# Kernel tuning notes

Hardware: AMD Instinct MI355X
Metric: run time of the kernel (lower is better)

## Reference

```python
import jax, jax.numpy as jnp
import numpy as np
from math import sqrt

ALPHA = 1.0
EPS = 1e-8


def setup_inputs() -> dict:
    key = jax.random.key(0)
    k1, k2, k3 = jax.random.split(key, 3)
    B, L, S, H, E = 4, 2048, 2048, 16, 64
    queries = jax.random.normal(k1, (B, L, H, E), dtype=jnp.float32)
    keys = jax.random.normal(k2, (B, S, H, E), dtype=jnp.float32)
    values = jax.random.normal(k3, (B, S, H, E), dtype=jnp.float32)
    return {"queries": queries, "keys": keys, "values": values}


def reference(queries, keys, values):
    B, L, H, E = queries.shape
    scale = 1.0 / sqrt(E)
    # dot product scores: [B,H,L,S]
    dot = jnp.einsum('blhe,bshe->bhls', queries, keys)
    # squared norms: [B,H,L,1] and [B,H,1,S]
    qn2 = jnp.sum(queries * queries, axis=-1).transpose(0, 2, 1)[..., :, None]
    kn2 = jnp.sum(keys * keys, axis=-1).transpose(0, 2, 1)[..., None, :]
    # wedge (parallelogram area) norm^2 = |q|^2|k|^2 - (q.k)^2, clipped at 0
    wedge_norm = jnp.sqrt(jax.nn.relu(qn2 * kn2 - dot * dot) + EPS)
    scores = ((1.0 - ALPHA) * dot + ALPHA * wedge_norm) * scale
    A = jax.nn.softmax(scores, axis=-1)  # no mask (mask_flag=False), dropout=0
    V = jnp.einsum('bhls,bshd->blhd', A, values)
    return V, jnp.mean(jnp.abs(scores))
```

## Files before the change

kernel.cpp:

```cpp
#include <hip/hip_runtime.h>
#include <math.h>

constexpr int Bb = 4, Ll = 2048, Ss = 2048, Hh = 16, Ee = 64;
constexpr float SCALE = 0.125f;
constexpr float EPSV  = 1e-8f;
constexpr float S2E   = 0.125f * 1.44269504089f;
constexpr float INV_CNT = 1.0f / (4.0f * 16.0f * 2048.0f * 2048.0f);

typedef __attribute__((ext_vector_type(8))) short  short8;
typedef __attribute__((ext_vector_type(4))) float  floatx4;

#define MFMA __builtin_amdgcn_mfma_f32_16x16x32_bf16

#define GLL(gp, lp)                                                        \
  __builtin_amdgcn_global_load_lds(                                        \
      (const __attribute__((address_space(1))) unsigned int*)(gp),         \
      (__attribute__((address_space(3))) unsigned int*)(lp), 16, 0, 0)

__device__ __forceinline__ short f2bf(float f) {
  unsigned u = __builtin_bit_cast(unsigned, f);
  u += 0x7fffu + ((u >> 16) & 1u);
  return (short)(u >> 16);
}
__device__ __forceinline__ float sq4(float4 v) {
  return v.x * v.x + v.y * v.y + v.z * v.z + v.w * v.w;
}
__device__ __forceinline__ short8 pack8(float4 x, float4 y) {
  short8 r;
  r[0] = f2bf(x.x); r[1] = f2bf(x.y); r[2] = f2bf(x.z); r[3] = f2bf(x.w);
  r[4] = f2bf(y.x); r[5] = f2bf(y.y); r[6] = f2bf(y.z); r[7] = f2bf(y.w);
  return r;
}

__global__ __launch_bounds__(256) void geom_pre_kernel(
    const float* __restrict__ Kg, const float* __restrict__ Vg,
    short* __restrict__ Kbf, short* __restrict__ Vtg,
    float* __restrict__ kn2g, float* __restrict__ sumg) {
  __shared__ short Vl[64][72];
  const int tid = threadIdx.x;
  const int bid = blockIdx.x;
  const int st = bid & 31, h = (bid >> 5) & 15, b = bid >> 9;
  const int s0 = st * 64;
  const int r64 = tid >> 2, ec = (tid & 3) * 16;
  const int bh = b * 16 + h;

  if (bid == 0 && tid == 0) *sumg = 0.0f;

  const float4* kp = (const float4*)(Kg + (((size_t)b * Ss + s0 + r64) * Hh + h) * Ee + ec);
  float4 k0 = kp[0], k1 = kp[1], k2 = kp[2], k3 = kp[3];
  float kn = sq4(k0) + sq4(k1) + sq4(k2) + sq4(k3);
  kn += __shfl_xor(kn, 1);
  kn += __shfl_xor(kn, 2);
  if ((tid & 3) == 0) kn2g[(size_t)bh * Ss + s0 + r64] = kn;
  short* ko = Kbf + ((size_t)bh * Ss + s0 + r64) * Ee + ec;
  *(short8*)(ko)     = pack8(k0, k1);
  *(short8*)(ko + 8) = pack8(k2, k3);

  const float4* vp = (const float4*)(Vg + (((size_t)b * Ss + s0 + r64) * Hh + h) * Ee + ec);
  float4 v0 = vp[0], v1 = vp[1], v2 = vp[2], v3 = vp[3];
  *(short8*)(&Vl[r64][ec])     = pack8(v0, v1);
  *(short8*)(&Vl[r64][ec + 8]) = pack8(v2, v3);
  __syncthreads();
  const int e = tid >> 2, sc = (tid & 3) * 16;
  short8 t0, t1;
#pragma unroll
  for (int j = 0; j < 8; ++j) {
    t0[j] = Vl[sc + j][e];
    t1[j] = Vl[sc + 8 + j][e];
  }
  short* vo = Vtg + ((size_t)bh * Ee + e) * Ss + s0 + sc;
  *(short8*)(vo)     = t0;
  *(short8*)(vo + 8) = t1;
}

constexpr int VOFF = 8192, POFF = 16384, KNOFF = 25600, LWOFF = 33792, RDOFF = 34048;

__global__ __launch_bounds__(256, 4) void geom_attn_kernel(
    const float* __restrict__ Qg, const short* __restrict__ Kbf,
    const short* __restrict__ Vtg, const float* __restrict__ kn2g,
    float* __restrict__ outg, float* __restrict__ sumg) {
  __shared__ __align__(16) char smem[34064];

  const int tid  = threadIdx.x;
  const int w    = tid >> 6;
  const int lane = tid & 63;
  const int c    = lane & 15;
  const int q4   = lane >> 4;

  const int bid = blockIdx.x;
  const int lt = bid & 31, h = (bid >> 5) & 15, b = bid >> 9;
  const int l0 = lt * 64 + w * 16;
  const int bh = b * 16 + h;

  const float4* qp = (const float4*)(Qg + (((size_t)b * Ll + (l0 + c)) * Hh + h) * Ee);
  float4 a0 = qp[2 * q4], a1 = qp[2 * q4 + 1];
  float4 a2 = qp[8 + 2 * q4], a3 = qp[9 + 2 * q4];
  float qn = sq4(a0) + sq4(a1) + sq4(a2) + sq4(a3);
  qn += __shfl_xor(qn, 16);
  qn += __shfl_xor(qn, 32);
  const float qn2v = qn;
  short8 qb0 = pack8(a0, a1);
  short8 qb1 = pack8(a2, a3);

  const int Gl = w * 128 + lane;
  const int rK = Gl >> 3, pK = Gl & 7;
  const int gK = pK ^ (rK & 7);
  const char* kSrc = (const char*)Kbf + (size_t)bh * Ss * 128 + rK * 128 + gK * 16;
  const char* vSrc = (const char*)Vtg + (size_t)bh * Ee * 4096 + rK * 4096 + gK * 16;
  char* kDst = smem + w * 2048;
  char* vDst = smem + VOFF + w * 2048;

  {
    const char* knSrc = (const char*)kn2g + (size_t)bh * 8192 + (w * 128 + lane) * 16;
    char* knDst = smem + KNOFF + w * 2048;
    GLL(knSrc, knDst);
    GLL(knSrc + 1024, knDst + 1024);
  }

  const int addrA0 = c * 128 + ((q4 ^ (c & 7)) << 4);
  const int addrA1 = addrA0 ^ 64;
  const char* pKa0 = smem + addrA0;
  const char* pKa1 = smem + addrA1;
  char* pPw  = smem + POFF + w * 2304;
  char* pPwr = pPw + c * 144 + q4 * 8;
  const char* pPrd = pPw + c * 144;
  const char* pKn  = smem + KNOFF + q4 * 16;
  float* lw = (float*)(smem + LWOFF + w * 64);
  float* red = (float*)(smem + RDOFF);

  floatx4 o0 = {0.f, 0.f, 0.f, 0.f}, o1 = o0, o2 = o0, o3 = o0;
  float lp = 0.0f, scsum = 0.0f;

  for (int s0 = 0; s0 < Ss; s0 += 64) {
    __syncthreads();
    GLL(kSrc, kDst);
    GLL(kSrc + 1024, kDst + 1024);
    GLL(vSrc, vDst);
    GLL(vSrc + 32768, vDst + 1024);
    kSrc += 8192;
    vSrc += 128;
    __syncthreads();

#pragma unroll
    for (int ct = 0; ct < 4; ++ct) {
      short8 ka0 = *(const short8*)(pKa0 + ct * 2048);
      short8 ka1 = *(const short8*)(pKa1 + ct * 2048);
      floatx4 d = {0.f, 0.f, 0.f, 0.f};
      d = MFMA(ka0, qb0, d, 0, 0, 0);
      d = MFMA(ka1, qb1, d, 0, 0, 0);
      float4 knv = *(const float4*)(pKn + s0 * 4 + ct * 64);
      float p[4];
#pragma unroll
      for (int r = 0; r < 4; ++r) {
        float dot = d[r];
        float w2 = fmaf(-dot, dot, qn2v * (&knv.x)[r]);
        w2 = fmaxf(w2, 0.0f) + EPSV;
        float rt = __builtin_amdgcn_sqrtf(w2);
        scsum += rt * SCALE;
        float pe = __builtin_amdgcn_exp2f(rt * S2E);
        lp += pe;
        p[r] = pe;
      }
      unsigned u0 = __builtin_bit_cast(unsigned, p[0]) + 0x8000u;
      unsigned u1 = __builtin_bit_cast(unsigned, p[1]) + 0x8000u;
      unsigned u2 = __builtin_bit_cast(unsigned, p[2]) + 0x8000u;
      unsigned u3 = __builtin_bit_cast(unsigned, p[3]) + 0x8000u;
      uint2 pk;
      pk.x = __builtin_amdgcn_perm(u1, u0, 0x07060302u);
      pk.y = __builtin_amdgcn_perm(u3, u2, 0x07060302u);
      *(uint2*)(pPwr + ct * 32) = pk;
    }

#pragma unroll
    for (int kc = 0; kc < 2; ++kc) {
      short8 pa = *(const short8*)(pPrd + kc * 64);
      const char* vb = (kc == 0 ? pKa0 : pKa1) + VOFF;
      short8 v0 = *(const short8*)(vb);
      short8 v1 = *(const short8*)(vb + 2048);
      short8 v2 = *(const short8*)(vb + 4096);
      short8 v3 = *(const short8*)(vb + 6144);
      o0 = MFMA(pa, v0, o0, 0, 0, 0);
      o1 = MFMA(pa, v1, o1, 0, 0, 0);
      o2 = MFMA(pa, v2, o2, 0, 0, 0);
      o3 = MFMA(pa, v3, o3, 0, 0, 0);
    }
  }

  lp += __shfl_xor(lp, 16);
  lp += __shfl_xor(lp, 32);
  if (lane < 16) lw[lane] = lp;
  __syncthreads();
  float4 lv = *(const float4*)((const char*)lw + q4 * 16);

#pragma unroll
  for (int r = 0; r < 4; ++r) {
    float inv = 1.0f / (&lv.x)[r];
    int row = l0 + q4 * 4 + r;
    float* orow = outg + (((size_t)b * Ll + row) * Hh + h) * Ee;
    orow[0 + c]  = o0[r] * inv;
    orow[16 + c] = o1[r] * inv;
    orow[32 + c] = o2[r] * inv;
    orow[48 + c] = o3[r] * inv;
  }

  scsum += __shfl_xor(scsum, 1);
  scsum += __shfl_xor(scsum, 2);
  scsum += __shfl_xor(scsum, 4);
  scsum += __shfl_xor(scsum, 8);
  scsum += __shfl_xor(scsum, 16);
  scsum += __shfl_xor(scsum, 32);
  if (lane == 0) red[w] = scsum;
  __syncthreads();
  if (tid == 0) {
    float s = red[0] + red[1] + red[2] + red[3];
    atomicAdd(sumg, s * INV_CNT);
  }
}

extern "C" void kernel_launch(void* const* d_in, const int* in_sizes, int n_in,
                              void* d_out, int out_size, void* d_ws, size_t ws_size,
                              hipStream_t stream) {
  const float* Q = (const float*)d_in[0];
  const float* K = (const float*)d_in[1];
  const float* V = (const float*)d_in[2];
  float* out   = (float*)d_out;
  float* sumsc = out + (size_t)Bb * Ll * Hh * Ee;

  short* Kbf = (short*)d_ws;
  short* Vtg = Kbf + (size_t)Bb * Hh * Ss * Ee;
  float* kn2 = (float*)(Vtg + (size_t)Bb * Hh * Ee * Ss);

  hipLaunchKernelGGL(geom_pre_kernel, dim3(Bb * Hh * (Ss / 64)), dim3(256), 0,
                     stream, K, V, Kbf, Vtg, kn2, sumsc);
  hipLaunchKernelGGL(geom_attn_kernel, dim3(Bb * Hh * (Ll / 64)), dim3(256), 0,
                     stream, Q, Kbf, Vtg, kn2, out, sumsc);
}
```

Baseline: 268.9 us.

## Drop LDS staging of key norms and raise attention kernel occupancy

The per-head key squared norms are no longer staged into shared memory; each lane reads them as float4 directly from global memory, which cuts the shared-memory footprint from about 34 KB to about 26 KB. Launch bounds rise from 4 to 6 blocks per CU so more waves can be resident. The inner loop is also trimmed: the clamp becomes a single max against EPS, the score scale is folded into the final atomic, and the bf16 packing of probabilities truncates instead of rounding. The read offset for the probability tile now includes a per-lane-group term, which also changes which probability columns each lane feeds into the PV matmul. Risks are extra global/L1 traffic for the norms, register pressure from the tighter occupancy bound, and slightly different bf16 rounding of the probabilities.

```diff
diff --git a/kernel.cpp b/kernel.cpp
--- a/kernel.cpp
+++ b/kernel.cpp
@@ -73,13 +73,13 @@
   *(short8*)(vo + 8) = t1;
 }
 
-constexpr int VOFF = 8192, POFF = 16384, KNOFF = 25600, LWOFF = 33792, RDOFF = 34048;
-
-__global__ __launch_bounds__(256, 4) void geom_attn_kernel(
+constexpr int VOFF = 8192, POFF = 16384, LWOFF = 25600, RDOFF = 25856;
+
+__global__ __launch_bounds__(256, 6) void geom_attn_kernel(
     const float* __restrict__ Qg, const short* __restrict__ Kbf,
     const short* __restrict__ Vtg, const float* __restrict__ kn2g,
     float* __restrict__ outg, float* __restrict__ sumg) {
-  __shared__ __align__(16) char smem[34064];
+  __shared__ __align__(16) char smem[25872];
 
   const int tid  = threadIdx.x;
   const int w    = tid >> 6;
@@ -110,12 +110,7 @@
   char* kDst = smem + w * 2048;
   char* vDst = smem + VOFF + w * 2048;
 
-  {
-    const char* knSrc = (const char*)kn2g + (size_t)bh * 8192 + (w * 128 + lane) * 16;
-    char* knDst = smem + KNOFF + w * 2048;
-    GLL(knSrc, knDst);
-    GLL(knSrc + 1024, knDst + 1024);
-  }
+  const float4* knp = (const float4*)(kn2g + (size_t)bh * Ss) + q4;
 
   const int addrA0 = c * 128 + ((q4 ^ (c & 7)) << 4);
   const int addrA1 = addrA0 ^ 64;
@@ -123,8 +118,7 @@
   const char* pKa1 = smem + addrA1;
   char* pPw  = smem + POFF + w * 2304;
   char* pPwr = pPw + c * 144 + q4 * 8;
-  const char* pPrd = pPw + c * 144;
-  const char* pKn  = smem + KNOFF + q4 * 16;
+  const char* pPrd = pPw + c * 144 + q4 * 16;
   float* lw = (float*)(smem + LWOFF + w * 64);
   float* red = (float*)(smem + RDOFF);
 
@@ -148,26 +142,24 @@
       floatx4 d = {0.f, 0.f, 0.f, 0.f};
       d = MFMA(ka0, qb0, d, 0, 0, 0);
       d = MFMA(ka1, qb1, d, 0, 0, 0);
-      float4 knv = *(const float4*)(pKn + s0 * 4 + ct * 64);
+      float4 knv = knp[(s0 >> 2) + ct * 4];
       float p[4];
 #pragma unroll
       for (int r = 0; r < 4; ++r) {
         float dot = d[r];
         float w2 = fmaf(-dot, dot, qn2v * (&knv.x)[r]);
-        w2 = fmaxf(w2, 0.0f) + EPSV;
+        w2 = fmaxf(w2, EPSV);
         float rt = __builtin_amdgcn_sqrtf(w2);
-        scsum += rt * SCALE;
+        scsum += rt;
         float pe = __builtin_amdgcn_exp2f(rt * S2E);
         lp += pe;
         p[r] = pe;
       }
-      unsigned u0 = __builtin_bit_cast(unsigned, p[0]) + 0x8000u;
-      unsigned u1 = __builtin_bit_cast(unsigned, p[1]) + 0x8000u;
-      unsigned u2 = __builtin_bit_cast(unsigned, p[2]) + 0x8000u;
-      unsigned u3 = __builtin_bit_cast(unsigned, p[3]) + 0x8000u;
       uint2 pk;
-      pk.x = __builtin_amdgcn_perm(u1, u0, 0x07060302u);
-      pk.y = __builtin_amdgcn_perm(u3, u2, 0x07060302u);
+      pk.x = __builtin_amdgcn_perm(__builtin_bit_cast(unsigned, p[1]),
+                                   __builtin_bit_cast(unsigned, p[0]), 0x07060302u);
+      pk.y = __builtin_amdgcn_perm(__builtin_bit_cast(unsigned, p[3]),
+                                   __builtin_bit_cast(unsigned, p[2]), 0x07060302u);
       *(uint2*)(pPwr + ct * 32) = pk;
     }
 
@@ -213,7 +205,7 @@
   __syncthreads();
   if (tid == 0) {
     float s = red[0] + red[1] + red[2] + red[3];
-    atomicAdd(sumg, s * INV_CNT);
+    atomicAdd(sumg, s * (SCALE * INV_CNT));
   }
 }
 
```

Measured after the change: 273.8 us. Within noise of the previous version (+1.8%).
